# Optimization experiments

Measured on AMD Instinct MI355X. Metric: run time of the kernel, lower is better.

Reference implementation:

```python
import jax, jax.numpy as jnp
import numpy as np
import math

D_MODEL = 256; N_LEVELS = 5; N_HEADS = 8; N_POINTS = 4
D_HEAD = D_MODEL // N_HEADS
BS = 1; T = 5; H = 64; W = 96


def conv3x3(x, w, b):
    # x: (N, C, H, W), w: (O, C, 3, 3) -> SAME padding conv
    y = jax.lax.conv_general_dilated(x, w, (1, 1), ((1, 1), (1, 1)),
                                     dimension_numbers=('NCHW', 'OIHW', 'NCHW'))
    return y + b[None, :, None, None]


def bilinear_zero(img, px, py):
    # img: (C, Hh, Ww); px, py: (...) pixel coords; zero padding outside.
    C, Hh, Ww = img.shape
    x0 = jnp.floor(px); y0 = jnp.floor(py)
    wx1 = px - x0; wx0 = 1.0 - wx1
    wy1 = py - y0; wy0 = 1.0 - wy1

    def gather(xi, yi):
        valid = (xi >= 0) & (xi < Ww) & (yi >= 0) & (yi < Hh)
        xc = jnp.clip(xi, 0, Ww - 1).astype(jnp.int32)
        yc = jnp.clip(yi, 0, Hh - 1).astype(jnp.int32)
        return img[:, yc, xc] * valid.astype(img.dtype)

    return (gather(x0, y0) * (wx0 * wy0) + gather(x0 + 1, y0) * (wx1 * wy0)
            + gather(x0, y0 + 1) * (wx0 * wy1) + gather(x0 + 1, y0 + 1) * (wx1 * wy1))


def warp(x, flo):
    # x: (b, c, h, w), flo: (b, 2, h, w); grid_sample(align_corners=True) equivalent
    b, c, h, w = x.shape
    gy, gx = jnp.meshgrid(jnp.arange(h, dtype=x.dtype), jnp.arange(w, dtype=x.dtype), indexing='ij')
    px = gx[None] + flo[:, 0]
    py = gy[None] + flo[:, 1]
    return jax.vmap(bilinear_zero)(x, px, py)


def flow_guid_offset(ff, fb, offset):
    # ff, fb: (b, 4, 2, h, w); offset: (N, T*h*w, heads, L, P, 2)
    N, THW, heads, L, P, _ = offset.shape
    hw = THW // L
    off = offset.reshape(N, L, hw, heads, L, P, 2)
    f01, f12, f23, f34 = ff[:, 0], ff[:, 1], ff[:, 2], ff[:, 3]
    f02 = f01 + warp(f12, f01)
    f03 = f02 + warp(f23, f02)
    f04 = f03 + warp(f34, f03)
    f13 = f12 + warp(f23, f12)
    f14 = f13 + warp(f34, f13)
    f24 = f23 + warp(f34, f23)
    b10, b21, b32, b43 = fb[:, 0], fb[:, 1], fb[:, 2], fb[:, 3]
    b42 = b43 + warp(b32, b43)
    b41 = b42 + warp(b21, b42)
    b40 = b41 + warp(b10, b41)
    b31 = b32 + warp(b21, b32)
    b30 = b31 + warp(b10, b31)
    b20 = b21 + warp(b10, b21)

    def flat(f):  # (b, 2, h, w) -> (b, hw, 2)
        return f.transpose(0, 2, 3, 1).reshape(f.shape[0], -1, 2)

    z = jnp.zeros_like(flat(f01))
    adds = jnp.stack([
        jnp.stack([z, flat(f01), flat(f02), flat(f03), flat(f04)], axis=2),
        jnp.stack([flat(b10), z, flat(f12), flat(f13), flat(f14)], axis=2),
        jnp.stack([flat(b20), flat(b21), z, flat(f23), flat(f24)], axis=2),
        jnp.stack([flat(b30), flat(b31), flat(b32), z, flat(f34)], axis=2),
        # NOTE: source repeats chunk3's flows for chunk4 (kept faithfully)
        jnp.stack([flat(b30), flat(b31), flat(b32), z, flat(f34)], axis=2),
    ], axis=1)  # (b, L, hw, L, 2)
    off = off + adds[:, :, :, None, :, None, :]
    return off.reshape(N, THW, heads, L, P, 2)


def _forward(query, input_flatten, reference_points, input_spatial_shapes,
             input_level_start_index, input_padding_mask, flow_forward, flow_backward,
             w_off, b_off, w_attn, b_attn, w_val, b_val, w_out, b_out):
    bs, t, c, h, w = query.shape
    q2 = query.reshape(bs * t, c, h, w)
    value = conv3x3(input_flatten.reshape(bs * t, c, h, w), w_val, b_val)
    off = conv3x3(q2, w_off, b_off)      # (bs*t, heads*L*P*2, h, w)
    aw = conv3x3(q2, w_attn, b_attn)     # (bs*t, heads*L*P, h, w)
    Lq = t * h * w

    def to_tokens(x):  # (bs*t, C, h, w) -> (bs, t*h*w, C)
        return x.reshape(bs, t, -1, h * w).transpose(0, 1, 3, 2).reshape(bs, Lq, -1)

    value = to_tokens(value)
    off = to_tokens(off)
    aw = to_tokens(aw)
    value = jnp.where(input_padding_mask[..., None], jnp.zeros((), value.dtype), value)
    value = value.reshape(bs, Lq, N_HEADS, D_HEAD)
    off = off.reshape(bs, Lq, N_HEADS, N_LEVELS, N_POINTS, 2)
    off = flow_guid_offset(flow_forward, flow_backward, off)
    aw = jax.nn.softmax(aw.reshape(bs, Lq, N_HEADS, N_LEVELS * N_POINTS), axis=-1)
    aw = aw.reshape(bs, Lq, N_HEADS, N_LEVELS, N_POINTS)
    # sampling locations, normalized by (W_l, H_l)
    normalizer = jnp.stack([input_spatial_shapes[:, 1], input_spatial_shapes[:, 0]], -1).astype(off.dtype)
    loc = reference_points[:, :, None, :, None, :] + off / normalizer[None, None, None, :, None, :]
    # core: multi-scale deformable bilinear sampling (grid_sample align_corners=False)
    value_lvl = value.reshape(bs, t, h * w, N_HEADS, D_HEAD)
    out = jnp.zeros((bs * N_HEADS, D_HEAD, Lq), dtype=value.dtype)
    for lvl in range(N_LEVELS):
        v = value_lvl[:, lvl].reshape(bs, h, w, N_HEADS, D_HEAD)
        v = v.transpose(0, 3, 4, 1, 2).reshape(bs * N_HEADS, D_HEAD, h, w)
        l = loc[:, :, :, lvl]  # (bs, Lq, heads, P, 2)
        px = (l[..., 0] * w - 0.5).transpose(0, 2, 1, 3).reshape(bs * N_HEADS, Lq, N_POINTS)
        py = (l[..., 1] * h - 0.5).transpose(0, 2, 1, 3).reshape(bs * N_HEADS, Lq, N_POINTS)
        samp = jax.vmap(bilinear_zero)(v, px, py)  # (bs*heads, D_HEAD, Lq, P)
        w_l = aw[:, :, :, lvl].transpose(0, 2, 1, 3).reshape(bs * N_HEADS, 1, Lq, N_POINTS)
        out = out + jnp.sum(samp * w_l, axis=-1)
    out = out.reshape(bs, N_HEADS, D_HEAD, Lq).transpose(0, 3, 1, 2).reshape(bs, Lq, c)
    out = out.reshape(bs, t, h * w, c).transpose(0, 1, 3, 2).reshape(bs * t, c, h, w)
    out = conv3x3(out, w_out, b_out)
    return out.reshape(bs, t, c, h, w)


def setup_inputs() -> dict:
    key = jax.random.key(0)
    ks = jax.random.split(key, 10)
    Lq = T * H * W
    query = jax.random.normal(ks[0], (BS, T, D_MODEL, H, W), jnp.float32)
    input_flatten = jax.random.normal(ks[1], (BS, T, D_MODEL, H, W), jnp.float32)
    reference_points = jax.random.uniform(ks[2], (BS, Lq, N_LEVELS, 2), jnp.float32)
    input_spatial_shapes = jnp.tile(jnp.array([[H, W]], jnp.int32), (N_LEVELS, 1))
    input_level_start_index = jnp.arange(N_LEVELS, dtype=jnp.int32) * (H * W)
    input_padding_mask = jnp.zeros((BS, Lq), dtype=bool)
    flow_forward = jax.random.normal(ks[3], (BS, 4, 2, H, W), jnp.float32) * 2.0
    flow_backward = jax.random.normal(ks[4], (BS, 4, 2, H, W), jnp.float32) * 2.0

    def xavier(k, shape):
        fan_in = shape[1] * shape[2] * shape[3]
        fan_out = shape[0] * shape[2] * shape[3]
        lim = math.sqrt(6.0 / (fan_in + fan_out))
        return jax.random.uniform(k, shape, jnp.float32, -lim, lim)

    w_off = jax.random.normal(ks[5], (N_HEADS * N_LEVELS * N_POINTS * 2, D_MODEL, 3, 3), jnp.float32) * 0.01
    # bias init follows _reset_parameters grid_init
    thetas = np.arange(N_HEADS) * (2.0 * np.pi / N_HEADS)
    grid = np.stack([np.cos(thetas), np.sin(thetas)], -1)
    grid = grid / np.abs(grid).max(-1, keepdims=True)
    grid = np.tile(grid.reshape(N_HEADS, 1, 1, 2), (1, N_LEVELS, N_POINTS, 1))
    for i in range(N_POINTS):
        grid[:, :, i, :] *= i + 1
    b_off = jnp.asarray(grid.reshape(-1), jnp.float32)
    w_attn = jax.random.normal(ks[6], (N_HEADS * N_LEVELS * N_POINTS, D_MODEL, 3, 3), jnp.float32) * 0.01
    b_attn = jnp.zeros((N_HEADS * N_LEVELS * N_POINTS,), jnp.float32)
    w_val = xavier(ks[7], (D_MODEL, D_MODEL, 3, 3)); b_val = jnp.zeros((D_MODEL,), jnp.float32)
    w_out = xavier(ks[8], (D_MODEL, D_MODEL, 3, 3)); b_out = jnp.zeros((D_MODEL,), jnp.float32)
    return {"query": query, "input_flatten": input_flatten, "reference_points": reference_points,
            "input_spatial_shapes": input_spatial_shapes, "input_level_start_index": input_level_start_index,
            "input_padding_mask": input_padding_mask, "flow_forward": flow_forward, "flow_backward": flow_backward,
            "w_off": w_off, "b_off": b_off, "w_attn": w_attn, "b_attn": b_attn,
            "w_val": w_val, "b_val": b_val, "w_out": w_out, "b_out": b_out}


def reference(query, input_flatten, reference_points, input_spatial_shapes,
              input_level_start_index, input_padding_mask, flow_forward, flow_backward,
              w_off, b_off, w_attn, b_attn, w_val, b_val, w_out, b_out):
    return _forward(query, input_flatten, reference_points, input_spatial_shapes,
                    input_level_start_index, input_padding_mask, flow_forward, flow_backward,
                    w_off, b_off, w_attn, b_attn, w_val, b_val, w_out, b_out)
```

## Files before the change

kernel.cpp:

```cpp
#include <hip/hip_runtime.h>
#include <hip/hip_bf16.h>
#include <hip/hip_fp16.h>

typedef __hip_bfloat16 bf16;
typedef __attribute__((ext_vector_type(8))) short short8;
typedef __attribute__((ext_vector_type(4))) float float4v;

#define T_  5
#define H_  64
#define W_  96
#define HW_ (H_*W_)
#define C_  256
#define NH_ 8
#define DH_ 32
#define NL_ 5
#define NP_ 4
#define LQ_ (T_*HW_)
#define UNITS_ (LQ_*NH_)

#define PH_ 66
#define PW_ 98

static __device__ __forceinline__ void gl2lds16(const bf16* g, bf16* l){
  __builtin_amdgcn_global_load_lds(
      (const __attribute__((address_space(1))) unsigned int*)g,
      (__attribute__((address_space(3))) unsigned int*)l, 16, 0, 0);
}

static __device__ __forceinline__ float bilin2(const float* __restrict__ img,
                                               float px, float py){
  float x0f = floorf(px), y0f = floorf(py);
  int x0 = (int)x0f, y0 = (int)y0f;
  float fx = px - x0f, fy = py - y0f;
  int x1 = x0+1, y1 = y0+1;
  bool vx0 = (x0>=0)&&(x0<W_), vx1 = (x1>=0)&&(x1<W_);
  bool vy0 = (y0>=0)&&(y0<H_), vy1 = (y1>=0)&&(y1<H_);
  float c00 = (vx0&&vy0)? img[y0*W_+x0] : 0.f;
  float c10 = (vx1&&vy0)? img[y0*W_+x1] : 0.f;
  float c01 = (vx0&&vy1)? img[y1*W_+x0] : 0.f;
  float c11 = (vx1&&vy1)? img[y1*W_+x1] : 0.f;
  return c00*(1.f-fx)*(1.f-fy) + c10*fx*(1.f-fy) + c01*(1.f-fx)*fy + c11*fx*fy;
}

#define MG_PAD   960
#define MG_WT    1025
#define MG_INIT  336
#define MG_FA    120
#define MG_BZ    405
__global__ __launch_bounds__(256) void mega0_k(
    const float* __restrict__ in0, const float* __restrict__ in1,
    bf16* __restrict__ pad0, bf16* __restrict__ pad1,
    const float* __restrict__ wv, const float* __restrict__ wo,
    const float* __restrict__ wa, const float* __restrict__ wout,
    const float* __restrict__ bo, const float* __restrict__ ba,
    bf16* __restrict__ WTv, bf16* __restrict__ WToa, bf16* __restrict__ WTout,
    float* __restrict__ boa,
    const float* __restrict__ ff, const float* __restrict__ fb,
    float* __restrict__ flows)
{
  __shared__ __align__(16) char smem[33792];
  int b = blockIdx.x, tid = threadIdx.x;
  if (b < MG_PAD){
    bf16 (*sb)[66] = (bf16(*)[66])smem;
    int z = b / 480, r = b - z*480;
    int t = r / 96, bxp = r - t*96;
    const float* in = z ? in1 : in0;
    bf16* pad       = z ? pad1 : pad0;
    int pix0 = bxp*64;
    int pl = tid & 63, cg = tid >> 6;
    #pragma unroll 4
    for (int it=0; it<64; ++it){
      int c = it*4 + cg;
      sb[c][pl] = __float2bfloat16(in[((size_t)t*C_ + c)*HW_ + pix0 + pl]);
    }
    __syncthreads();
    for (int p=0; p<64; ++p){
      int pix = pix0 + p;
      int y = pix/W_, x = pix - y*W_;
      pad[(((size_t)t*PH_ + y+1)*PW_ + x+1)*C_ + tid] = sb[tid][p];
    }
    return;
  }
  b -= MG_PAD;
  if (b < MG_WT){
    if (b == 1024){
      #pragma unroll
      for (int k=0;k<2;++k){
        int n = tid + k*256;
        float v = 0.f;
        if (n < 320) v = bo[n]; else if (n < 480) v = ba[n-320];
        boa[n] = v;
      }
      return;
    }
    float* ld = (float*)smem;
    const float* src; bf16* dst;
    if (b < 256){ src = wv + (size_t)b*2304; dst = WTv + (size_t)b*2304; }
    else if (b < 768){
      int n = b-256; dst = WToa + (size_t)n*2304;
      src = (n<320) ? (wo + (size_t)n*2304)
          : ((n<480) ? (wa + (size_t)(n-320)*2304) : (const float*)0);
    } else { int n = b-768; src = wout + (size_t)n*2304; dst = WTout + (size_t)n*2304; }
    if (src){
      #pragma unroll
      for (int k=0;k<9;++k) ld[tid + k*256] = src[tid + k*256];
      __syncthreads();
      #pragma unroll
      for (int k=0;k<9;++k){
        int o = tid + k*256; int tap = o >> 8, ci = o & 255;
        dst[o] = __float2bfloat16(ld[ci*9 + tap]);
      }
    } else {
      #pragma unroll
      for (int k=0;k<9;++k) dst[tid + k*256] = __float2bfloat16(0.f);
    }
    return;
  }
  b -= MG_WT;
  if (b < MG_INIT){
    int i = b*256 + tid;
    const int per = 2*HW_;
    int f = i/per, r = i - f*per;
    if (f < 4) flows[f*per + r]          = ff[i];
    else       flows[(10+(f-4))*per + r] = fb[(f-4)*per + r];
    return;
  }
  b -= MG_INIT;
  if (b < MG_FA){
    int ci = b / 24;
    int pix = (b - ci*24)*256 + tid;
    const int dsts[5] = {4,7,9,13,14};
    const float* A; const float* S;
    switch(ci){
      case 0: A = ff;          S = ff + 2*HW_; break;
      case 1: A = ff + 2*HW_;  S = ff + 4*HW_; break;
      case 2: A = ff + 4*HW_;  S = ff + 6*HW_; break;
      case 3: A = fb + 2*HW_;  S = fb;         break;
      default:A = fb + 4*HW_;  S = fb + 2*HW_; break;
    }
    float* D = flows + dsts[ci]*2*HW_;
    float ax = A[pix], ay = A[HW_+pix];
    float px = (float)(pix % W_) + ax;
    float py = (float)(pix / W_) + ay;
    D[pix]      = ax + bilin2(S,      px, py);
    D[HW_+pix]  = ay + bilin2(S+HW_,  px, py);
    return;
  }
  b -= MG_FA;
  {
    int idx = b*256 + tid;
    int pair = idx / 10368, r = idx - pair*10368;
    int pxi = r >> 5, q8 = r & 31;
    int t = pair >> 1, z = pair & 1;
    int y, x;
    if (pxi < 98){ y = 0;  x = pxi; }
    else if (pxi < 196){ y = 65; x = pxi-98; }
    else if (pxi < 260){ y = pxi-196+1; x = 0; }
    else { y = pxi-260+1; x = 97; }
    bf16* pad = z ? pad1 : pad0;
    uint4 zz; zz.x = zz.y = zz.z = zz.w = 0u;
    *(uint4*)(pad + (((size_t)t*PH_ + y)*PW_ + x)*C_ + q8*8) = zz;
  }
}

__global__ __launch_bounds__(256) void flowBC_k(const float* __restrict__ ff,
                                                const float* __restrict__ fb,
                                                float* __restrict__ flows){
  int gy = blockIdx.y;
  int pix = blockIdx.x*256 + threadIdx.x;
  float gx = (float)(pix % W_), gyy = (float)(pix / W_);
  if (gy == 0){
    const float* A   = flows + 4*2*HW_;
    const float* S23 = ff + 4*HW_;
    const float* S34 = ff + 6*HW_;
    float ax = A[pix], ay = A[HW_+pix];
    float px = gx + ax, py = gyy + ay;
    float c3x = ax + bilin2(S23,      px, py);
    float c3y = ay + bilin2(S23+HW_,  px, py);
    float* D3 = flows + 5*2*HW_;
    D3[pix] = c3x; D3[HW_+pix] = c3y;
    px = gx + c3x; py = gyy + c3y;
    float* D4 = flows + 6*2*HW_;
    D4[pix]     = c3x + bilin2(S34,     px, py);
    D4[HW_+pix] = c3y + bilin2(S34+HW_, px, py);
  } else if (gy == 1){
    const float* A = flows + 7*2*HW_;
    const float* S = ff + 6*HW_;
    float ax = A[pix], ay = A[HW_+pix];
    float px = gx + ax, py = gyy + ay;
    float* D = flows + 8*2*HW_;
    D[pix]     = ax + bilin2(S,     px, py);
    D[HW_+pix] = ay + bilin2(S+HW_, px, py);
  } else {
    const float* A = flows + 14*2*HW_;
    const float* S = fb;
    float ax = A[pix], ay = A[HW_+pix];
    float px = gx + ax, py = gyy + ay;
    float* D = flows + 15*2*HW_;
    D[pix]     = ax + bilin2(S,     px, py);
    D[HW_+pix] = ay + bilin2(S+HW_, px, py);
  }
}

#define BM 128
#define BN 256
#define BK 64

__global__ __launch_bounds__(256,2) void gemm12_k(const bf16* __restrict__ Av,
                                                  const bf16* __restrict__ Aq,
                                                  const bf16* __restrict__ WTv,
                                                  const bf16* __restrict__ WToa,
                                                  const float* __restrict__ bv,
                                                  const float* __restrict__ boa,
                                                  bf16* __restrict__ outv,
                                                  float* __restrict__ P,
                                                  float* __restrict__ aw){
  __shared__ __align__(16) bf16 As[BM*BK];
  __shared__ __align__(16) bf16 Bs[BN*BK];
  int tid = threadIdx.x;
  int lane = tid & 63, wvi = tid >> 6;
  int wm = wvi & 1, wn = wvi >> 1;
  int quad = lane >> 4, l15 = lane & 15;
  int bx = blockIdx.x, byy = blockIdx.y;
  bool isval = byy == 0;
  const bf16* Apad  = isval ? Av  : Aq;
  const bf16* WT    = isval ? WTv : WToa;
  const float* bias = isval ? bv  : boa;
  int nby = isval ? 0 : byy - 1;

  int srow = tid >> 3;
  int c8   = (tid & 7) ^ (srow & 7);
  long abase[4];
  #pragma unroll
  for (int j=0;j<4;++j){
    int p = j*32 + srow;
    int Pm = bx*BM + p;
    int t = Pm / HW_, rem = Pm - t*HW_;
    int y = rem / W_, x = rem - y*W_;
    abase[j] = ((long)(t*PH_ + y)*PW_ + x)*C_ + c8*8;
  }
  const bf16* bbase = WT + (size_t)(nby*BN + srow)*2304 + c8*8;

  float4v acc[4][8];
  #pragma unroll
  for (int jn=0;jn<8;++jn){
    float bvv = bias[nby*BN + wn*128 + jn*16 + l15];
    #pragma unroll
    for (int i=0;i<4;++i){ acc[i][jn][0]=bvv; acc[i][jn][1]=bvv; acc[i][jn][2]=bvv; acc[i][jn][3]=bvv; }
  }

  for (int kt=0; kt<36; ++kt){
    int tap = kt >> 2, kc = (kt & 3) << 6;
    int dy = tap/3, dx = tap - dy*3;
    long ash = (long)(dy*PW_ + dx)*C_ + kc;
    long bsh = (long)kt*64;
    __syncthreads();
    #pragma unroll
    for (int j=0;j<4;++j)
      gl2lds16(Apad + abase[j] + ash, As + (j*256+tid)*8);
    #pragma unroll
    for (int j=0;j<8;++j)
      gl2lds16(bbase + (size_t)j*32*2304 + bsh, Bs + (j*256+tid)*8);
    __syncthreads();
    #pragma unroll
    for (int kk=0; kk<2; ++kk){
      int slot = ((kk<<2) + quad) ^ (l15 & 7);
      short8 af[4], bfr[8];
      #pragma unroll
      for (int jn=0;jn<8;++jn)
        bfr[jn] = *(const short8*)(Bs + (wn*128 + jn*16 + l15)*BK + slot*8);
      #pragma unroll
      for (int i=0;i<4;++i)
        af[i] = *(const short8*)(As + (wm*64 + i*16 + l15)*BK + slot*8);
      #pragma unroll
      for (int i=0;i<4;++i)
        #pragma unroll
        for (int jn=0;jn<8;++jn)
          acc[i][jn] = __builtin_amdgcn_mfma_f32_16x16x32_bf16(af[i], bfr[jn], acc[i][jn], 0,0,0);
    }
  }

  #pragma unroll
  for (int i=0;i<4;++i){
    int mr = bx*BM + wm*64 + i*16 + quad*4;
    #pragma unroll
    for (int jn=0;jn<8;++jn){
      int nc = nby*BN + wn*128 + jn*16 + l15;
      #pragma unroll
      for (int r=0;r<4;++r){
        float v = acc[i][jn][r];
        long m = mr + r;
        if (isval){
          outv[m*256 + nc] = __float2bfloat16(v);
        } else {
          if (nc < 320){
            int h = nc/40, rr = nc - h*40;
            int l = rr >> 3, pxy = rr & 7;
            P[((size_t)l*UNITS_ + m*8 + h)*8 + pxy] = v;
          } else if (nc < 480){
            int hh = (nc-320)/20, ii = (nc-320) - hh*20;
            aw[((size_t)m*8 + hh)*20 + ii] = v;
          }
        }
      }
    }
  }
}

__global__ __launch_bounds__(256,2) void gemm_out_k(const bf16* __restrict__ Apad,
                                                    const bf16* __restrict__ WT,
                                                    const float* __restrict__ bias,
                                                    float* __restrict__ out){
  __shared__ __align__(16) bf16 As[BM*BK];
  __shared__ __align__(16) bf16 Bs[BN*BK];
  int tid = threadIdx.x;
  int lane = tid & 63, wvi = tid >> 6;
  int wm = wvi & 1, wn = wvi >> 1;
  int quad = lane >> 4, l15 = lane & 15;
  int bx = blockIdx.x;

  int srow = tid >> 3;
  int c8   = (tid & 7) ^ (srow & 7);
  long abase[4];
  #pragma unroll
  for (int j=0;j<4;++j){
    int p = j*32 + srow;
    int Pm = bx*BM + p;
    int t = Pm / HW_, rem = Pm - t*HW_;
    int y = rem / W_, x = rem - y*W_;
    abase[j] = ((long)(t*PH_ + y)*PW_ + x)*C_ + c8*8;
  }
  const bf16* bbase = WT + (size_t)srow*2304 + c8*8;

  float4v acc[4][8];
  #pragma unroll
  for (int jn=0;jn<8;++jn){
    float bvv = bias[wn*128 + jn*16 + l15];
    #pragma unroll
    for (int i=0;i<4;++i){ acc[i][jn][0]=bvv; acc[i][jn][1]=bvv; acc[i][jn][2]=bvv; acc[i][jn][3]=bvv; }
  }

  for (int kt=0; kt<36; ++kt){
    int tap = kt >> 2, kc = (kt & 3) << 6;
    int dy = tap/3, dx = tap - dy*3;
    long ash = (long)(dy*PW_ + dx)*C_ + kc;
    long bsh = (long)kt*64;
    __syncthreads();
    #pragma unroll
    for (int j=0;j<4;++j)
      gl2lds16(Apad + abase[j] + ash, As + (j*256+tid)*8);
    #pragma unroll
    for (int j=0;j<8;++j)
      gl2lds16(bbase + (size_t)j*32*2304 + bsh, Bs + (j*256+tid)*8);
    __syncthreads();
    #pragma unroll
    for (int kk=0; kk<2; ++kk){
      int slot = ((kk<<2) + quad) ^ (l15 & 7);
      short8 af[4], bfr[8];
      #pragma unroll
      for (int jn=0;jn<8;++jn)
        bfr[jn] = *(const short8*)(Bs + (wn*128 + jn*16 + l15)*BK + slot*8);
      #pragma unroll
      for (int i=0;i<4;++i)
        af[i] = *(const short8*)(As + (wm*64 + i*16 + l15)*BK + slot*8);
      #pragma unroll
      for (int i=0;i<4;++i)
        #pragma unroll
        for (int jn=0;jn<8;++jn)
          acc[i][jn] = __builtin_amdgcn_mfma_f32_16x16x32_bf16(af[i], bfr[jn], acc[i][jn], 0,0,0);
    }
  }

  int t = (bx*BM) / HW_;
  #pragma unroll
  for (int i=0;i<4;++i){
    int m = bx*BM + wm*64 + i*16 + quad*4;
    int pix = m - t*HW_;
    #pragma unroll
    for (int jn=0;jn<8;++jn){
      int nc = wn*128 + jn*16 + l15;
      *(float4v*)(out + ((size_t)(t*C_ + nc))*HW_ + pix) = acc[i][jn];
    }
  }
}

__device__ const int g_slotTab[25] = {
  -1,  0,  4,  5,  6,
  10, -1,  1,  7,  8,
  13, 11, -1,  2,  9,
  15, 14, 12, -1,  3,
  15, 14, 12, -1,  3 };

__global__ __launch_bounds__(256) void prep_k(const float* __restrict__ aw,
                                              __half* __restrict__ w16){
  int unit = blockIdx.x*256 + threadIdx.x;
  const float4* p4 = (const float4*)(aw + (size_t)unit*20);
  float4 v[5];
  #pragma unroll
  for (int i=0;i<5;++i) v[i] = p4[i];
  float* e = (float*)v;
  float m = -1e30f;
  #pragma unroll
  for (int i=0;i<20;++i) m = fmaxf(m, e[i]);
  float s = 0.f;
  #pragma unroll
  for (int i=0;i<20;++i){ e[i] = __expf(e[i]-m); s += e[i]; }
  float inv = 1.f/s;
  __half2* o2 = (__half2*)(w16 + (size_t)unit*20);
  #pragma unroll
  for (int i=0;i<10;++i)
    o2[i] = __floats2half2_rn(e[2*i]*inv, e[2*i+1]*inv);
}

template<bool FIRST, bool LAST>
__global__ __launch_bounds__(256) void phase_k(const unsigned* __restrict__ vimg0,
                                               const float2*  __restrict__ Pl,
                                               const __half*  __restrict__ wl,
                                               const float*   __restrict__ ref,
                                               const float*   __restrict__ flows,
                                               int lvl,
                                               __half2* __restrict__ acc,
                                               bf16* __restrict__ attn_pad){
  __shared__ float4 sW[16][4];
  __shared__ int4   sI[16][4];
  int tid = threadIdx.x;
  if (tid < 64){
    int g = tid >> 2, p = tid & 3;
    int unit = blockIdx.x*16 + g;
    float2 pr = Pl[(size_t)unit*4 + p];
    float w = __half2float(wl[(size_t)unit*20 + p]);
    int q = unit >> 3;
    int t_q = q / HW_, pix = q - t_q*HW_;
    int slot = g_slotTab[t_q*5 + lvl];
    float ax = 0.f, ay = 0.f;
    if (slot >= 0){ ax = flows[slot*2*HW_ + pix]; ay = flows[slot*2*HW_ + HW_ + pix]; }
    float ppx = pr.x + ref[(q*5+lvl)*2+0]*(float)W_ - 0.5f + ax;
    float ppy = pr.y + ref[(q*5+lvl)*2+1]*(float)H_ - 0.5f + ay;
    float x0f = floorf(ppx), y0f = floorf(ppy);
    float fx = ppx - x0f,    fy = ppy - y0f;
    int x0 = (int)x0f, y0 = (int)y0f;
    int x1 = x0+1, y1 = y0+1;
    float wx0 = 1.f-fx, wx1 = fx, wy0 = 1.f-fy, wy1 = fy;
    if ((unsigned)x0 >= (unsigned)W_) wx0 = 0.f;
    if ((unsigned)x1 >= (unsigned)W_) wx1 = 0.f;
    if ((unsigned)y0 >= (unsigned)H_) wy0 = 0.f;
    if ((unsigned)y1 >= (unsigned)H_) wy1 = 0.f;
    int xc0 = min(max(x0,0),W_-1), xc1 = min(max(x1,0),W_-1);
    int yc0 = min(max(y0,0),H_-1), yc1 = min(max(y1,0),H_-1);
    sW[g][p] = make_float4(w*wx0*wy0, w*wx1*wy0, w*wx0*wy1, w*wx1*wy1);
    sI[g][p] = make_int4((yc0*W_+xc0)*128, (yc0*W_+xc1)*128,
                         (yc1*W_+xc0)*128, (yc1*W_+xc1)*128);
  }
  __syncthreads();
  int g = tid >> 4, e = tid & 15;
  int unit = blockIdx.x*16 + g;
  int q = unit >> 3, h = unit & 7;
  const unsigned* vimg = vimg0 + h*16 + e;
  float a0, a1;
  if (FIRST){ a0 = 0.f; a1 = 0.f; }
  else { __half2 c = acc[(size_t)unit*16 + e]; a0 = __low2float(c); a1 = __high2float(c); }
  #pragma unroll
  for (int p=0; p<4; ++p){
    float4 w4 = sW[g][p];
    int4   i4 = sI[g][p];
    unsigned u00 = vimg[i4.x], u10 = vimg[i4.y];
    unsigned u01 = vimg[i4.z], u11 = vimg[i4.w];
    union {unsigned v; float f;} lo, hi;
    lo.v = u00<<16; hi.v = u00 & 0xffff0000u;
    a0 = fmaf(w4.x, lo.f, a0); a1 = fmaf(w4.x, hi.f, a1);
    lo.v = u10<<16; hi.v = u10 & 0xffff0000u;
    a0 = fmaf(w4.y, lo.f, a0); a1 = fmaf(w4.y, hi.f, a1);
    lo.v = u01<<16; hi.v = u01 & 0xffff0000u;
    a0 = fmaf(w4.z, lo.f, a0); a1 = fmaf(w4.z, hi.f, a1);
    lo.v = u11<<16; hi.v = u11 & 0xffff0000u;
    a0 = fmaf(w4.w, lo.f, a0); a1 = fmaf(w4.w, hi.f, a1);
  }
  if (LAST){
    int t_q = q / HW_, pix = q - t_q*HW_;
    int yq = pix / W_, xq = pix - yq*W_;
    union {unsigned u; bf16 hh[2];} pk;
    pk.hh[0] = __float2bfloat16(a0);
    pk.hh[1] = __float2bfloat16(a1);
    *(unsigned*)(attn_pad + (((size_t)t_q*PH_ + yq+1)*PW_ + xq+1)*C_ + h*DH_ + e*2) = pk.u;
  } else {
    acc[(size_t)unit*16 + e] = __floats2half2_rn(a0, a1);
  }
}

extern "C" void kernel_launch(void* const* d_in, const int* in_sizes, int n_in,
                              void* d_out, int out_size, void* d_ws, size_t ws_size,
                              hipStream_t stream) {
  const float* query   = (const float*)d_in[0];
  const float* in_flat = (const float*)d_in[1];
  const float* refpts  = (const float*)d_in[2];
  const float* ff      = (const float*)d_in[6];
  const float* fb      = (const float*)d_in[7];
  const float* w_off   = (const float*)d_in[8];
  const float* b_off   = (const float*)d_in[9];
  const float* w_attn  = (const float*)d_in[10];
  const float* b_attn  = (const float*)d_in[11];
  const float* w_val   = (const float*)d_in[12];
  const float* b_val   = (const float*)d_in[13];
  const float* w_out   = (const float*)d_in[14];
  const float* b_out   = (const float*)d_in[15];
  float* out = (float*)d_out;

  char* ws = (char*)d_ws;
  bf16*  v_pad   = (bf16*) (ws + 0);
  bf16*  q_pad   = (bf16*) (ws + 16558080);
  __half* w16    = (__half*)(ws + 16558080);
  bf16*  v_val   = (bf16*) (ws + 33116160);
  float* P       = (float*)(ws + 48844800);
  float* v_aw    = (float*)(ws + 88166400);
  __half2* acc   = (__half2*)(ws + 88166400);
  float* v_flows = (float*)(ws + 107827200);
  bf16*  WT_val  = (bf16*) (ws + 108613632);
  bf16*  WT_oa   = (bf16*) (ws + 109793280);
  bf16*  WT_out  = (bf16*) (ws + 112152576);
  float* bias_oa = (float*)(ws + 113332224);
  bf16*  attn_pad = v_pad;
  if (ws_size < (size_t)113334272) return;

  mega0_k<<<MG_PAD+MG_WT+MG_INIT+MG_FA+MG_BZ, 256, 0, stream>>>(
      in_flat, query, v_pad, q_pad,
      w_val, w_off, w_attn, w_out, b_off, b_attn,
      WT_val, WT_oa, WT_out, bias_oa, ff, fb, v_flows);

  flowBC_k<<<dim3(HW_/256, 3), 256, 0, stream>>>(ff, fb, v_flows);

  gemm12_k<<<dim3(240, 3), 256, 0, stream>>>(v_pad, q_pad, WT_val, WT_oa,
                                             b_val, bias_oa, v_val, P, v_aw);

  prep_k<<<UNITS_/256, 256, 0, stream>>>(v_aw, w16);

  {
    const unsigned* vb = (const unsigned*)v_val;
    phase_k<true ,false><<<UNITS_/16, 256, 0, stream>>>(vb + 0ul*HW_*128,
        (const float2*)(P + 0ul*UNITS_*8), w16 + 0,  refpts, v_flows, 0, acc, attn_pad);
    phase_k<false,false><<<UNITS_/16, 256, 0, stream>>>(vb + 1ul*HW_*128,
        (const float2*)(P + 1ul*UNITS_*8), w16 + 4,  refpts, v_flows, 1, acc, attn_pad);
    phase_k<false,false><<<UNITS_/16, 256, 0, stream>>>(vb + 2ul*HW_*128,
        (const float2*)(P + 2ul*UNITS_*8), w16 + 8,  refpts, v_flows, 2, acc, attn_pad);
    phase_k<false,false><<<UNITS_/16, 256, 0, stream>>>(vb + 3ul*HW_*128,
        (const float2*)(P + 3ul*UNITS_*8), w16 + 12, refpts, v_flows, 3, acc, attn_pad);
    phase_k<false,true ><<<UNITS_/16, 256, 0, stream>>>(vb + 4ul*HW_*128,
        (const float2*)(P + 4ul*UNITS_*8), w16 + 16, refpts, v_flows, 4, acc, attn_pad);
  }

  gemm_out_k<<<dim3(240, 1), 256, 0, stream>>>(attn_pad, WT_out, b_out, out);
}
```

Measured before the change: 451.9 us.

## Triple-buffer LDS with async prefetch in conv GEMMs and use eight waves

Both implicit-GEMM conv kernels now use three LDS stages. Tiles two K-steps ahead are issued with global_load_lds and gated by explicit vmcnt waits, replacing the old load-then-compute loop that put two syncthreads around every K-step. The block grows to 512 threads (8 waves), each owning a 64x64 output sub-tile instead of 64x128, which halves per-wave accumulator registers. The cost is about 144KB of LDS per block, which limits each CU to one resident block, plus hand-tuned waitcnt counts that must match the number of loads issued per stage.

```diff
diff --git a/kernel.cpp b/kernel.cpp
--- a/kernel.cpp
+++ b/kernel.cpp
@@ -206,7 +206,7 @@
 #define BN 256
 #define BK 64
 
-__global__ __launch_bounds__(256,2) void gemm12_k(const bf16* __restrict__ Av,
+__global__ __launch_bounds__(512,2) void gemm12_k(const bf16* __restrict__ Av,
                                                   const bf16* __restrict__ Aq,
                                                   const bf16* __restrict__ WTv,
                                                   const bf16* __restrict__ WToa,
@@ -215,8 +215,8 @@
                                                   bf16* __restrict__ outv,
                                                   float* __restrict__ P,
                                                   float* __restrict__ aw){
-  __shared__ __align__(16) bf16 As[BM*BK];
-  __shared__ __align__(16) bf16 Bs[BN*BK];
+  __shared__ __align__(16) bf16 As[3][BM*BK];
+  __shared__ __align__(16) bf16 Bs[3][BN*BK];
   int tid = threadIdx.x;
   int lane = tid & 63, wvi = tid >> 6;
   int wm = wvi & 1, wn = wvi >> 1;
@@ -230,62 +230,83 @@
 
   int srow = tid >> 3;
   int c8   = (tid & 7) ^ (srow & 7);
-  long abase[4];
-  #pragma unroll
-  for (int j=0;j<4;++j){
-    int p = j*32 + srow;
+  long abase[2];
+  #pragma unroll
+  for (int r=0;r<2;++r){
+    int p = r*64 + srow;
     int Pm = bx*BM + p;
     int t = Pm / HW_, rem = Pm - t*HW_;
     int y = rem / W_, x = rem - y*W_;
-    abase[j] = ((long)(t*PH_ + y)*PW_ + x)*C_ + c8*8;
+    abase[r] = ((long)(t*PH_ + y)*PW_ + x)*C_ + c8*8;
   }
   const bf16* bbase = WT + (size_t)(nby*BN + srow)*2304 + c8*8;
 
-  float4v acc[4][8];
-  #pragma unroll
-  for (int jn=0;jn<8;++jn){
-    float bvv = bias[nby*BN + wn*128 + jn*16 + l15];
+  float4v acc[4][4];
+  #pragma unroll
+  for (int jn=0;jn<4;++jn){
+    float bvv = bias[nby*BN + wn*64 + jn*16 + l15];
     #pragma unroll
     for (int i=0;i<4;++i){ acc[i][jn][0]=bvv; acc[i][jn][1]=bvv; acc[i][jn][2]=bvv; acc[i][jn][3]=bvv; }
   }
-
-  for (int kt=0; kt<36; ++kt){
-    int tap = kt >> 2, kc = (kt & 3) << 6;
+  asm volatile("s_waitcnt vmcnt(0)" ::: "memory");
+  __builtin_amdgcn_sched_barrier(0);
+
+  auto stage = [&](int kt_, int sl){
+    int tap = kt_ >> 2, kc = (kt_ & 3) << 6;
     int dy = tap/3, dx = tap - dy*3;
     long ash = (long)(dy*PW_ + dx)*C_ + kc;
-    long bsh = (long)kt*64;
-    __syncthreads();
+    long bsh = (long)kt_*64;
+    gl2lds16(Apad + abase[0] + ash, &As[sl][(size_t)(0*512+tid)*8]);
+    gl2lds16(Apad + abase[1] + ash, &As[sl][(size_t)(1*512+tid)*8]);
     #pragma unroll
     for (int j=0;j<4;++j)
-      gl2lds16(Apad + abase[j] + ash, As + (j*256+tid)*8);
-    #pragma unroll
-    for (int j=0;j<8;++j)
-      gl2lds16(bbase + (size_t)j*32*2304 + bsh, Bs + (j*256+tid)*8);
-    __syncthreads();
+      gl2lds16(bbase + (size_t)j*64*2304 + bsh, &Bs[sl][(size_t)(j*512+tid)*8]);
+  };
+
+  stage(0,0);
+  stage(1,1);
+  for (int kt=0; kt<36; ++kt){
+    int s = kt % 3;
+    if (kt < 34){
+      stage(kt+2, (kt+2)%3);
+      asm volatile("s_waitcnt vmcnt(12)" ::: "memory");
+    } else if (kt == 34){
+      asm volatile("s_waitcnt vmcnt(6)" ::: "memory");
+    } else {
+      asm volatile("s_waitcnt vmcnt(0)" ::: "memory");
+    }
+    __builtin_amdgcn_sched_barrier(0);
+    __builtin_amdgcn_s_barrier();
+    __builtin_amdgcn_sched_barrier(0);
+    const bf16* Asl = &As[s][0];
+    const bf16* Bsl = &Bs[s][0];
     #pragma unroll
     for (int kk=0; kk<2; ++kk){
       int slot = ((kk<<2) + quad) ^ (l15 & 7);
-      short8 af[4], bfr[8];
-      #pragma unroll
-      for (int jn=0;jn<8;++jn)
-        bfr[jn] = *(const short8*)(Bs + (wn*128 + jn*16 + l15)*BK + slot*8);
+      short8 af[4], bfr[4];
+      #pragma unroll
+      for (int jn=0;jn<4;++jn)
+        bfr[jn] = *(const short8*)(Bsl + (wn*64 + jn*16 + l15)*BK + slot*8);
       #pragma unroll
       for (int i=0;i<4;++i)
-        af[i] = *(const short8*)(As + (wm*64 + i*16 + l15)*BK + slot*8);
+        af[i] = *(const short8*)(Asl + (wm*64 + i*16 + l15)*BK + slot*8);
       #pragma unroll
       for (int i=0;i<4;++i)
         #pragma unroll
-        for (int jn=0;jn<8;++jn)
+        for (int jn=0;jn<4;++jn)
           acc[i][jn] = __builtin_amdgcn_mfma_f32_16x16x32_bf16(af[i], bfr[jn], acc[i][jn], 0,0,0);
     }
+    __builtin_amdgcn_sched_barrier(0);
+    __builtin_amdgcn_s_barrier();
+    __builtin_amdgcn_sched_barrier(0);
   }
 
   #pragma unroll
   for (int i=0;i<4;++i){
     int mr = bx*BM + wm*64 + i*16 + quad*4;
     #pragma unroll
-    for (int jn=0;jn<8;++jn){
-      int nc = nby*BN + wn*128 + jn*16 + l15;
+    for (int jn=0;jn<4;++jn){
+      int nc = nby*BN + wn*64 + jn*16 + l15;
       #pragma unroll
       for (int r=0;r<4;++r){
         float v = acc[i][jn][r];
@@ -307,12 +328,12 @@
   }
 }
 
-__global__ __launch_bounds__(256,2) void gemm_out_k(const bf16* __restrict__ Apad,
+__global__ __launch_bounds__(512,2) void gemm_out_k(const bf16* __restrict__ Apad,
                                                     const bf16* __restrict__ WT,
                                                     const float* __restrict__ bias,
                                                     float* __restrict__ out){
-  __shared__ __align__(16) bf16 As[BM*BK];
-  __shared__ __align__(16) bf16 Bs[BN*BK];
+  __shared__ __align__(16) bf16 As[3][BM*BK];
+  __shared__ __align__(16) bf16 Bs[3][BN*BK];
   int tid = threadIdx.x;
   int lane = tid & 63, wvi = tid >> 6;
   int wm = wvi & 1, wn = wvi >> 1;
@@ -321,54 +342,75 @@
 
   int srow = tid >> 3;
   int c8   = (tid & 7) ^ (srow & 7);
-  long abase[4];
-  #pragma unroll
-  for (int j=0;j<4;++j){
-    int p = j*32 + srow;
+  long abase[2];
+  #pragma unroll
+  for (int r=0;r<2;++r){
+    int p = r*64 + srow;
     int Pm = bx*BM + p;
     int t = Pm / HW_, rem = Pm - t*HW_;
     int y = rem / W_, x = rem - y*W_;
-    abase[j] = ((long)(t*PH_ + y)*PW_ + x)*C_ + c8*8;
+    abase[r] = ((long)(t*PH_ + y)*PW_ + x)*C_ + c8*8;
   }
   const bf16* bbase = WT + (size_t)srow*2304 + c8*8;
 
-  float4v acc[4][8];
-  #pragma unroll
-  for (int jn=0;jn<8;++jn){
-    float bvv = bias[wn*128 + jn*16 + l15];
+  float4v acc[4][4];
+  #pragma unroll
+  for (int jn=0;jn<4;++jn){
+    float bvv = bias[wn*64 + jn*16 + l15];
     #pragma unroll
     for (int i=0;i<4;++i){ acc[i][jn][0]=bvv; acc[i][jn][1]=bvv; acc[i][jn][2]=bvv; acc[i][jn][3]=bvv; }
   }
-
-  for (int kt=0; kt<36; ++kt){
-    int tap = kt >> 2, kc = (kt & 3) << 6;
+  asm volatile("s_waitcnt vmcnt(0)" ::: "memory");
+  __builtin_amdgcn_sched_barrier(0);
+
+  auto stage = [&](int kt_, int sl){
+    int tap = kt_ >> 2, kc = (kt_ & 3) << 6;
     int dy = tap/3, dx = tap - dy*3;
     long ash = (long)(dy*PW_ + dx)*C_ + kc;
-    long bsh = (long)kt*64;
-    __syncthreads();
+    long bsh = (long)kt_*64;
+    gl2lds16(Apad + abase[0] + ash, &As[sl][(size_t)(0*512+tid)*8]);
+    gl2lds16(Apad + abase[1] + ash, &As[sl][(size_t)(1*512+tid)*8]);
     #pragma unroll
     for (int j=0;j<4;++j)
-      gl2lds16(Apad + abase[j] + ash, As + (j*256+tid)*8);
-    #pragma unroll
-    for (int j=0;j<8;++j)
-      gl2lds16(bbase + (size_t)j*32*2304 + bsh, Bs + (j*256+tid)*8);
-    __syncthreads();
+      gl2lds16(bbase + (size_t)j*64*2304 + bsh, &Bs[sl][(size_t)(j*512+tid)*8]);
+  };
+
+  stage(0,0);
+  stage(1,1);
+  for (int kt=0; kt<36; ++kt){
+    int s = kt % 3;
+    if (kt < 34){
+      stage(kt+2, (kt+2)%3);
+      asm volatile("s_waitcnt vmcnt(12)" ::: "memory");
+    } else if (kt == 34){
+      asm volatile("s_waitcnt vmcnt(6)" ::: "memory");
+    } else {
+      asm volatile("s_waitcnt vmcnt(0)" ::: "memory");
+    }
+    __builtin_amdgcn_sched_barrier(0);
+    __builtin_amdgcn_s_barrier();
+    __builtin_amdgcn_sched_barrier(0);
+    const bf16* Asl = &As[s][0];
+    const bf16* Bsl = &Bs[s][0];
     #pragma unroll
     for (int kk=0; kk<2; ++kk){
       int slot = ((kk<<2) + quad) ^ (l15 & 7);
-      short8 af[4], bfr[8];
-      #pragma unroll
-      for (int jn=0;jn<8;++jn)
-        bfr[jn] = *(const short8*)(Bs + (wn*128 + jn*16 + l15)*BK + slot*8);
+      short8 af[4], bfr[4];
+      #pragma unroll
+      for (int jn=0;jn<4;++jn)
+        bfr[jn] = *(const short8*)(Bsl + (wn*64 + jn*16 + l15)*BK + slot*8);
       #pragma unroll
       for (int i=0;i<4;++i)
-        af[i] = *(const short8*)(As + (wm*64 + i*16 + l15)*BK + slot*8);
+        af[i] = *(const short8*)(Asl + (wm*64 + i*16 + l15)*BK + slot*8);
       #pragma unroll
       for (int i=0;i<4;++i)
         #pragma unroll
-        for (int jn=0;jn<8;++jn)
+        for (int jn=0;jn<4;++jn)
           acc[i][jn] = __builtin_amdgcn_mfma_f32_16x16x32_bf16(af[i], bfr[jn], acc[i][jn], 0,0,0);
     }
+    __builtin_amdgcn_sched_barrier(0);
+    __builtin_amdgcn_s_barrier();
+    __builtin_amdgcn_sched_barrier(0);
   }
 
   int t = (bx*BM) / HW_;
@@ -377,8 +419,8 @@
     int m = bx*BM + wm*64 + i*16 + quad*4;
     int pix = m - t*HW_;
     #pragma unroll
-    for (int jn=0;jn<8;++jn){
-      int nc = wn*128 + jn*16 + l15;
+    for (int jn=0;jn<4;++jn){
+      int nc = wn*64 + jn*16 + l15;
       *(float4v*)(out + ((size_t)(t*C_ + nc))*HW_ + pix) = acc[i][jn];
     }
   }
@@ -528,7 +570,7 @@
 
   flowBC_k<<<dim3(HW_/256, 3), 256, 0, stream>>>(ff, fb, v_flows);
 
-  gemm12_k<<<dim3(240, 3), 256, 0, stream>>>(v_pad, q_pad, WT_val, WT_oa,
+  gemm12_k<<<dim3(240, 3), 512, 0, stream>>>(v_pad, q_pad, WT_val, WT_oa,
                                              b_val, bias_oa, v_val, P, v_aw);
 
   prep_k<<<UNITS_/256, 256, 0, stream>>>(v_aw, w16);
@@ -547,5 +589,5 @@
         (const float2*)(P + 4ul*UNITS_*8), w16 + 16, refpts, v_flows, 4, acc, attn_pad);
   }
 
-  gemm_out_k<<<dim3(240, 1), 256, 0, stream>>>(attn_pad, WT_out, b_out, out);
-}
+  gemm_out_k<<<240, 512, 0, stream>>>(attn_pad, WT_out, b_out, out);
+}
```

Result: slower. 471.2 us (+4.3%).

## Fuse softmax prep and five per-level sampling kernels into one sampler

Applied to the files above, without the earlier changes.

Replaces the separate softmax kernel and five per-level sampling launches with a single kernel. Each block computes the softmax weights for 128 units into shared memory, then loops over all levels, keeping the per-unit accumulators in registers. This removes the fp16 accumulator round-trips through global memory and five kernel launches. In exchange, each block now issues many __syncthreads (two per level per group), and the per-level working set of each block is much smaller, which may reduce latency hiding.

```diff
diff --git a/kernel.cpp b/kernel.cpp
--- a/kernel.cpp
+++ b/kernel.cpp
@@ -391,99 +391,107 @@
   15, 14, 12, -1,  3,
   15, 14, 12, -1,  3 };
 
-__global__ __launch_bounds__(256) void prep_k(const float* __restrict__ aw,
-                                              __half* __restrict__ w16){
-  int unit = blockIdx.x*256 + threadIdx.x;
-  const float4* p4 = (const float4*)(aw + (size_t)unit*20);
-  float4 v[5];
-  #pragma unroll
-  for (int i=0;i<5;++i) v[i] = p4[i];
-  float* e = (float*)v;
-  float m = -1e30f;
-  #pragma unroll
-  for (int i=0;i<20;++i) m = fmaxf(m, e[i]);
-  float s = 0.f;
-  #pragma unroll
-  for (int i=0;i<20;++i){ e[i] = __expf(e[i]-m); s += e[i]; }
-  float inv = 1.f/s;
-  __half2* o2 = (__half2*)(w16 + (size_t)unit*20);
-  #pragma unroll
-  for (int i=0;i<10;++i)
-    o2[i] = __floats2half2_rn(e[2*i]*inv, e[2*i+1]*inv);
-}
-
-template<bool FIRST, bool LAST>
-__global__ __launch_bounds__(256) void phase_k(const unsigned* __restrict__ vimg0,
-                                               const float2*  __restrict__ Pl,
-                                               const __half*  __restrict__ wl,
-                                               const float*   __restrict__ ref,
-                                               const float*   __restrict__ flows,
-                                               int lvl,
-                                               __half2* __restrict__ acc,
-                                               bf16* __restrict__ attn_pad){
+#define SAMP_BLOCKS 1920
+#define GPB 8
+__global__ __launch_bounds__(256,8) void samp_k(const unsigned* __restrict__ vb,
+                                                const float*   __restrict__ P,
+                                                const float*   __restrict__ aw,
+                                                const float*   __restrict__ ref,
+                                                const float*   __restrict__ flows,
+                                                bf16* __restrict__ attn_pad){
+  __shared__ float  sWgt[128][20];
   __shared__ float4 sW[16][4];
   __shared__ int4   sI[16][4];
   int tid = threadIdx.x;
-  if (tid < 64){
-    int g = tid >> 2, p = tid & 3;
-    int unit = blockIdx.x*16 + g;
-    float2 pr = Pl[(size_t)unit*4 + p];
-    float w = __half2float(wl[(size_t)unit*20 + p]);
+  int u0 = blockIdx.x * (GPB*16);
+
+  if (tid < 128){
+    int unit = u0 + tid;
+    const float4* p4 = (const float4*)(aw + (size_t)unit*20);
+    float4 v[5];
+    #pragma unroll
+    for (int i=0;i<5;++i) v[i] = p4[i];
+    float* e = (float*)v;
+    float m = -1e30f;
+    #pragma unroll
+    for (int i=0;i<20;++i) m = fmaxf(m, e[i]);
+    float s = 0.f;
+    #pragma unroll
+    for (int i=0;i<20;++i){ e[i] = __expf(e[i]-m); s += e[i]; }
+    float inv = 1.f/s;
+    #pragma unroll
+    for (int i=0;i<20;++i) sWgt[tid][i] = e[i]*inv;
+  }
+
+  float a0[GPB], a1[GPB];
+  #pragma unroll
+  for (int j=0;j<GPB;++j){ a0[j]=0.f; a1[j]=0.f; }
+
+  int g = tid >> 4, e16 = tid & 15;
+  int h = g & 7;
+
+  for (int l=0; l<NL_; ++l){
+    const unsigned* vimg = vb + (size_t)l*HW_*128 + h*16 + e16;
+    #pragma unroll
+    for (int j=0;j<GPB;++j){
+      __syncthreads();
+      if (tid < 64){
+        int gg = tid >> 2, p = tid & 3;
+        int unit = u0 + j*16 + gg;
+        float2 pr = ((const float2*)P)[((size_t)l*UNITS_ + unit)*4 + p];
+        float w = sWgt[j*16+gg][l*4+p];
+        int q = unit >> 3;
+        int t_q = q / HW_, pix = q - t_q*HW_;
+        int slot = g_slotTab[t_q*5 + l];
+        float ax = 0.f, ay = 0.f;
+        if (slot >= 0){ ax = flows[slot*2*HW_ + pix]; ay = flows[slot*2*HW_ + HW_ + pix]; }
+        float ppx = pr.x + ref[(q*5+l)*2+0]*(float)W_ - 0.5f + ax;
+        float ppy = pr.y + ref[(q*5+l)*2+1]*(float)H_ - 0.5f + ay;
+        float x0f = floorf(ppx), y0f = floorf(ppy);
+        float fx = ppx - x0f,    fy = ppy - y0f;
+        int x0 = (int)x0f, y0 = (int)y0f;
+        int x1 = x0+1, y1 = y0+1;
+        float wx0 = 1.f-fx, wx1 = fx, wy0 = 1.f-fy, wy1 = fy;
+        if ((unsigned)x0 >= (unsigned)W_) wx0 = 0.f;
+        if ((unsigned)x1 >= (unsigned)W_) wx1 = 0.f;
+        if ((unsigned)y0 >= (unsigned)H_) wy0 = 0.f;
+        if ((unsigned)y1 >= (unsigned)H_) wy1 = 0.f;
+        int xc0 = min(max(x0,0),W_-1), xc1 = min(max(x1,0),W_-1);
+        int yc0 = min(max(y0,0),H_-1), yc1 = min(max(y1,0),H_-1);
+        sW[gg][p] = make_float4(w*wx0*wy0, w*wx1*wy0, w*wx0*wy1, w*wx1*wy1);
+        sI[gg][p] = make_int4((yc0*W_+xc0)*128, (yc0*W_+xc1)*128,
+                              (yc1*W_+xc0)*128, (yc1*W_+xc1)*128);
+      }
+      __syncthreads();
+      #pragma unroll
+      for (int p=0; p<4; ++p){
+        float4 w4 = sW[g][p];
+        int4   i4 = sI[g][p];
+        unsigned u00 = vimg[i4.x], u10 = vimg[i4.y];
+        unsigned u01 = vimg[i4.z], u11 = vimg[i4.w];
+        union {unsigned v; float f;} lo, hi;
+        lo.v = u00<<16; hi.v = u00 & 0xffff0000u;
+        a0[j] = fmaf(w4.x, lo.f, a0[j]); a1[j] = fmaf(w4.x, hi.f, a1[j]);
+        lo.v = u10<<16; hi.v = u10 & 0xffff0000u;
+        a0[j] = fmaf(w4.y, lo.f, a0[j]); a1[j] = fmaf(w4.y, hi.f, a1[j]);
+        lo.v = u01<<16; hi.v = u01 & 0xffff0000u;
+        a0[j] = fmaf(w4.z, lo.f, a0[j]); a1[j] = fmaf(w4.z, hi.f, a1[j]);
+        lo.v = u11<<16; hi.v = u11 & 0xffff0000u;
+        a0[j] = fmaf(w4.w, lo.f, a0[j]); a1[j] = fmaf(w4.w, hi.f, a1[j]);
+      }
+    }
+  }
+
+  #pragma unroll
+  for (int j=0;j<GPB;++j){
+    int unit = u0 + j*16 + g;
     int q = unit >> 3;
-    int t_q = q / HW_, pix = q - t_q*HW_;
-    int slot = g_slotTab[t_q*5 + lvl];
-    float ax = 0.f, ay = 0.f;
-    if (slot >= 0){ ax = flows[slot*2*HW_ + pix]; ay = flows[slot*2*HW_ + HW_ + pix]; }
-    float ppx = pr.x + ref[(q*5+lvl)*2+0]*(float)W_ - 0.5f + ax;
-    float ppy = pr.y + ref[(q*5+lvl)*2+1]*(float)H_ - 0.5f + ay;
-    float x0f = floorf(ppx), y0f = floorf(ppy);
-    float fx = ppx - x0f,    fy = ppy - y0f;
-    int x0 = (int)x0f, y0 = (int)y0f;
-    int x1 = x0+1, y1 = y0+1;
-    float wx0 = 1.f-fx, wx1 = fx, wy0 = 1.f-fy, wy1 = fy;
-    if ((unsigned)x0 >= (unsigned)W_) wx0 = 0.f;
-    if ((unsigned)x1 >= (unsigned)W_) wx1 = 0.f;
-    if ((unsigned)y0 >= (unsigned)H_) wy0 = 0.f;
-    if ((unsigned)y1 >= (unsigned)H_) wy1 = 0.f;
-    int xc0 = min(max(x0,0),W_-1), xc1 = min(max(x1,0),W_-1);
-    int yc0 = min(max(y0,0),H_-1), yc1 = min(max(y1,0),H_-1);
-    sW[g][p] = make_float4(w*wx0*wy0, w*wx1*wy0, w*wx0*wy1, w*wx1*wy1);
-    sI[g][p] = make_int4((yc0*W_+xc0)*128, (yc0*W_+xc1)*128,
-                         (yc1*W_+xc0)*128, (yc1*W_+xc1)*128);
-  }
-  __syncthreads();
-  int g = tid >> 4, e = tid & 15;
-  int unit = blockIdx.x*16 + g;
-  int q = unit >> 3, h = unit & 7;
-  const unsigned* vimg = vimg0 + h*16 + e;
-  float a0, a1;
-  if (FIRST){ a0 = 0.f; a1 = 0.f; }
-  else { __half2 c = acc[(size_t)unit*16 + e]; a0 = __low2float(c); a1 = __high2float(c); }
-  #pragma unroll
-  for (int p=0; p<4; ++p){
-    float4 w4 = sW[g][p];
-    int4   i4 = sI[g][p];
-    unsigned u00 = vimg[i4.x], u10 = vimg[i4.y];
-    unsigned u01 = vimg[i4.z], u11 = vimg[i4.w];
-    union {unsigned v; float f;} lo, hi;
-    lo.v = u00<<16; hi.v = u00 & 0xffff0000u;
-    a0 = fmaf(w4.x, lo.f, a0); a1 = fmaf(w4.x, hi.f, a1);
-    lo.v = u10<<16; hi.v = u10 & 0xffff0000u;
-    a0 = fmaf(w4.y, lo.f, a0); a1 = fmaf(w4.y, hi.f, a1);
-    lo.v = u01<<16; hi.v = u01 & 0xffff0000u;
-    a0 = fmaf(w4.z, lo.f, a0); a1 = fmaf(w4.z, hi.f, a1);
-    lo.v = u11<<16; hi.v = u11 & 0xffff0000u;
-    a0 = fmaf(w4.w, lo.f, a0); a1 = fmaf(w4.w, hi.f, a1);
-  }
-  if (LAST){
     int t_q = q / HW_, pix = q - t_q*HW_;
     int yq = pix / W_, xq = pix - yq*W_;
     union {unsigned u; bf16 hh[2];} pk;
-    pk.hh[0] = __float2bfloat16(a0);
-    pk.hh[1] = __float2bfloat16(a1);
-    *(unsigned*)(attn_pad + (((size_t)t_q*PH_ + yq+1)*PW_ + xq+1)*C_ + h*DH_ + e*2) = pk.u;
-  } else {
-    acc[(size_t)unit*16 + e] = __floats2half2_rn(a0, a1);
+    pk.hh[0] = __float2bfloat16(a0[j]);
+    pk.hh[1] = __float2bfloat16(a1[j]);
+    *(unsigned*)(attn_pad + (((size_t)t_q*PH_ + yq+1)*PW_ + xq+1)*C_ + h*DH_ + e16*2) = pk.u;
   }
 }
 
@@ -508,11 +516,9 @@
   char* ws = (char*)d_ws;
   bf16*  v_pad   = (bf16*) (ws + 0);
   bf16*  q_pad   = (bf16*) (ws + 16558080);
-  __half* w16    = (__half*)(ws + 16558080);
   bf16*  v_val   = (bf16*) (ws + 33116160);
   float* P       = (float*)(ws + 48844800);
   float* v_aw    = (float*)(ws + 88166400);
-  __half2* acc   = (__half2*)(ws + 88166400);
   float* v_flows = (float*)(ws + 107827200);
   bf16*  WT_val  = (bf16*) (ws + 108613632);
   bf16*  WT_oa   = (bf16*) (ws + 109793280);
@@ -531,21 +537,8 @@
   gemm12_k<<<dim3(240, 3), 256, 0, stream>>>(v_pad, q_pad, WT_val, WT_oa,
                                              b_val, bias_oa, v_val, P, v_aw);
 
-  prep_k<<<UNITS_/256, 256, 0, stream>>>(v_aw, w16);
-
-  {
-    const unsigned* vb = (const unsigned*)v_val;
-    phase_k<true ,false><<<UNITS_/16, 256, 0, stream>>>(vb + 0ul*HW_*128,
-        (const float2*)(P + 0ul*UNITS_*8), w16 + 0,  refpts, v_flows, 0, acc, attn_pad);
-    phase_k<false,false><<<UNITS_/16, 256, 0, stream>>>(vb + 1ul*HW_*128,
-        (const float2*)(P + 1ul*UNITS_*8), w16 + 4,  refpts, v_flows, 1, acc, attn_pad);
-    phase_k<false,false><<<UNITS_/16, 256, 0, stream>>>(vb + 2ul*HW_*128,
-        (const float2*)(P + 2ul*UNITS_*8), w16 + 8,  refpts, v_flows, 2, acc, attn_pad);
-    phase_k<false,false><<<UNITS_/16, 256, 0, stream>>>(vb + 3ul*HW_*128,
-        (const float2*)(P + 3ul*UNITS_*8), w16 + 12, refpts, v_flows, 3, acc, attn_pad);
-    phase_k<false,true ><<<UNITS_/16, 256, 0, stream>>>(vb + 4ul*HW_*128,
-        (const float2*)(P + 4ul*UNITS_*8), w16 + 16, refpts, v_flows, 4, acc, attn_pad);
-  }
+  samp_k<<<SAMP_BLOCKS, 256, 0, stream>>>((const unsigned*)v_val, P, v_aw,
+                                          refpts, v_flows, attn_pad);
 
   gemm_out_k<<<dim3(240, 1), 256, 0, stream>>>(attn_pad, WT_out, b_out, out);
 }
```

Result: slower. 576.6 us (+27.6%).
